# Performance work log

Hardware: AMD Instinct MI355X
Metric: run time of the kernel (lower is better)

The kernel has to match this reference:

```python
import jax, jax.numpy as jnp
import numpy as np

N_NODES = 50000
N_EDGES = 800000
D_IN = 128
D_OUT = 128


def setup_inputs() -> dict:
    key = jax.random.key(0)
    k1, k2, k3, k4 = jax.random.split(key, 4)
    feature = jax.random.normal(k1, (N_NODES, D_IN), dtype=jnp.float32)
    edge_src = jax.random.randint(k2, (N_EDGES,), 0, N_NODES, dtype=jnp.int32)
    edge_dst = jax.random.randint(k3, (N_EDGES,), 0, N_NODES, dtype=jnp.int32)
    W = jax.random.normal(k4, (D_IN, D_OUT), dtype=jnp.float32) * (1.0 / np.sqrt(D_IN))
    b = jnp.zeros((D_OUT,), dtype=jnp.float32)
    return {"feature": feature, "edge_src": edge_src, "edge_dst": edge_dst, "W": W, "b": b}


def reference(feature, edge_src, edge_dst, W, b):
    # copy_src + sum reduce: for each edge, copy src node feature, sum into dst node
    msgs = feature[edge_src]  # [E, D_IN] gather
    h = jax.ops.segment_sum(msgs, edge_dst, num_segments=N_NODES)  # [N, D_IN]
    # linear + activation (relu)
    return jax.nn.relu(h @ W + b)
```

## Files before the change

### kernel.cpp

```cpp
#include <hip/hip_runtime.h>
#include <hip/hip_fp16.h>


constexpr int N    = 50000;
constexpr int E    = 800000;
constexpr int D    = 128;
constexpr int CAP  = 64;
constexpr int NT   = 3125;
constexpr int ZSTR = 136;
constexpr int NR   = 782;
constexpr int HB   = 500;
constexpr int EPB  = E / HB;

using f16x8 = __attribute__((ext_vector_type(8))) _Float16;
using f32x4 = __attribute__((ext_vector_type(4))) float;

__global__ void setup(const float* __restrict__ W, _Float16* __restrict__ Wf,
                      _Float16* __restrict__ Z) {
    if (blockIdx.x == 8) {
        if (threadIdx.x < D) Z[(size_t)N * D + threadIdx.x] = (_Float16)0.f;
        return;
    }
    int t = blockIdx.x * 256 + threadIdx.x;
    int ct = t >> 8, ks = (t >> 6) & 3, lane = t & 63;
    int q = lane >> 4, li = lane & 15;
    _Float16 v[8];
    #pragma unroll
    for (int j = 0; j < 8; ++j)
        v[j] = (_Float16)W[(ks * 32 + q * 8 + j) * D + ct * 16 + li];
    *(f16x8*)(Wf + (size_t)t * 8) = *(const f16x8*)v;
}

__global__ __launch_bounds__(256) void midk(
        const float* __restrict__ feature,
        const int*   __restrict__ edst,
        const _Float16* __restrict__ Wf,
        int* __restrict__ hist,
        _Float16* __restrict__ Z) {
    __shared__ int h[NR];
    __shared__ _Float16 zs[4][16 * ZSTR];
    const int tid = threadIdx.x;

    if (blockIdx.x < HB) {
        const int b = blockIdx.x;
        for (int i = tid; i < NR; i += 256) h[i] = 0;
        __syncthreads();
        const int e0 = b * EPB;
        for (int i = tid; i < EPB; i += 256)
            atomicAdd(&h[edst[e0 + i] >> 6], 1);
        __syncthreads();
        for (int i = tid; i < NR; i += 256) hist[b * NR + i] = h[i];
        return;
    }

    const int wave = tid >> 6, lane = tid & 63;
    const int wt = (blockIdx.x - HB) * 4 + wave;
    if (wt >= NT) return;
    const int q = lane >> 4, li = lane & 15;

    const float* fp = feature + (size_t)(wt * 16 + li) * D + q * 8;
    f16x8 afr[4];
    #pragma unroll
    for (int ks = 0; ks < 4; ++ks) {
        const float4 u0 = *(const float4*)(fp + ks * 32);
        const float4 u1 = *(const float4*)(fp + ks * 32 + 4);
        afr[ks][0] = (_Float16)u0.x; afr[ks][1] = (_Float16)u0.y;
        afr[ks][2] = (_Float16)u0.z; afr[ks][3] = (_Float16)u0.w;
        afr[ks][4] = (_Float16)u1.x; afr[ks][5] = (_Float16)u1.y;
        afr[ks][6] = (_Float16)u1.z; afr[ks][7] = (_Float16)u1.w;
    }

    f32x4 acc[8];
    #pragma unroll
    for (int ct = 0; ct < 8; ++ct) acc[ct] = (f32x4){0.f, 0.f, 0.f, 0.f};
    #pragma unroll
    for (int ks = 0; ks < 4; ++ks)
        #pragma unroll
        for (int ct = 0; ct < 8; ++ct) {
            const f16x8 b = *(const f16x8*)(Wf + (size_t)((ct * 4 + ks) * 64 + lane) * 8);
            acc[ct] = __builtin_amdgcn_mfma_f32_16x16x32_f16(afr[ks], b, acc[ct], 0, 0, 0);
        }

    _Float16* zt = zs[wave];
    #pragma unroll
    for (int ct = 0; ct < 8; ++ct)
        #pragma unroll
        for (int r = 0; r < 4; ++r)
            zt[(q * 4 + r) * ZSTR + ct * 16 + li] = (_Float16)acc[ct][r];
    #pragma unroll
    for (int it = 0; it < 4; ++it) {
        const f16x8 v = *(const f16x8*)(zt + (it * 4 + q) * ZSTR + li * 8);
        *(f16x8*)(Z + (size_t)(wt * 16 + it * 4 + q) * D + li * 8) = v;
    }
}

__global__ void scank(int* __restrict__ hist, int* __restrict__ total) {
    const int r    = blockIdx.x;
    const int lane = threadIdx.x;
    int h[8], sum = 0;
    #pragma unroll
    for (int j = 0; j < 8; ++j) {
        const int idx = lane * 8 + j;
        h[j] = (idx < HB) ? hist[idx * NR + r] : 0;
        sum += h[j];
    }
    int incl = sum;
    #pragma unroll
    for (int off = 1; off < 64; off <<= 1) {
        int u = __shfl_up(incl, off);
        if (lane >= off) incl += u;
    }
    int run = incl - sum;
    #pragma unroll
    for (int j = 0; j < 8; ++j) {
        const int idx = lane * 8 + j;
        if (idx < HB) hist[idx * NR + r] = run;
        run += h[j];
    }
    if (lane == 63) total[r] = run;
}

__global__ __launch_bounds__(256) void partk(
        const int* __restrict__ esrc,
        const int* __restrict__ edst,
        const int* __restrict__ blockBase,
        const int* __restrict__ total,
        int* __restrict__ rangeStartG,
        unsigned int* __restrict__ part) {
    __shared__ int rs[NR];
    __shared__ int mb[NR];
    __shared__ int rk[NR];
    const int tid = threadIdx.x;
    const int b   = blockIdx.x;

    if (tid < 64) {
        int carry = 0;
        #pragma unroll
        for (int c = 0; c < 13; ++c) {
            const int idx = c * 64 + tid;
            const int v = (idx < NR) ? total[idx] : 0;
            int incl = v;
            #pragma unroll
            for (int off = 1; off < 64; off <<= 1) {
                int u = __shfl_up(incl, off);
                if (tid >= off) incl += u;
            }
            if (idx < NR) rs[idx] = incl - v + carry;
            carry += __shfl(incl, 63);
        }
    }
    for (int i = tid; i < NR; i += 256) { mb[i] = blockBase[b * NR + i]; rk[i] = 0; }
    __syncthreads();
    if (b == 0)
        for (int i = tid; i < NR; i += 256) rangeStartG[i] = rs[i];

    const int e0 = b * EPB;
    for (int i = tid; i < EPB; i += 256) {
        const int s = esrc[e0 + i];
        const int d = edst[e0 + i];
        const int r = d >> 6;
        const int k = atomicAdd(&rk[r], 1);
        part[rs[r] + mb[r] + k] = ((unsigned)(d & 63) << 16) | (unsigned)s;
    }
}

__global__ __launch_bounds__(256) void csrgather(
        const unsigned int* __restrict__ part,
        const int* __restrict__ rangeStart,
        const int* __restrict__ total,
        const _Float16* __restrict__ Z,
        const float* __restrict__ bias,
        float* __restrict__ out) {
    __shared__ unsigned short bkt[32 * CAP];
    __shared__ int deg[32];
    const int r   = blockIdx.x >> 1;
    const int sub = blockIdx.x & 1;
    const int tid = threadIdx.x;

    if (tid < 32) deg[tid] = 0;
    __syncthreads();
    const int rsv = rangeStart[r], tot = total[r];
    for (int i = tid; i < tot; i += 256) {
        const unsigned p = part[rsv + i];
        const int local = p >> 16;
        if ((local >> 5) == sub) {
            const int l5 = local & 31;
            const int k = atomicAdd(&deg[l5], 1);
            if (k < CAP) bkt[l5 * CAP + k] = (unsigned short)(p & 0xFFFF);
        }
    }
    __syncthreads();

    const int wave = tid >> 6, lane = tid & 63;
    const int g = lane >> 4, li = lane & 15;
    const float4 b0 = *(const float4*)(bias + li * 8);
    const float4 b1 = *(const float4*)(bias + li * 8 + 4);

    for (int pair = 0; pair < 4; ++pair) {
        const int lA = wave * 8 + pair * 2;
        const int lB = lA + 1;
        const int degA = min(deg[lA], CAP);
        const int degB = min(deg[lB], CAP);

        float accA[8] = {0,0,0,0,0,0,0,0};
        float accB[8] = {0,0,0,0,0,0,0,0};

        const int mx = max(degA, degB);
        for (int base = 0; base < mx; base += 16) {
            f16x8 hA[4], hB[4];
            #pragma unroll
            for (int t = 0; t < 4; ++t) {
                const int rr = base + t * 4 + g;
                int sA = bkt[lA * CAP + rr];
                int sB = bkt[lB * CAP + rr];
                sA = (rr < degA) ? sA : N;
                sB = (rr < degB) ? sB : N;
                hA[t] = *(const f16x8*)(Z + (size_t)sA * D + li * 8);
                hB[t] = *(const f16x8*)(Z + (size_t)sB * D + li * 8);
            }
            #pragma unroll
            for (int t = 0; t < 4; ++t)
                #pragma unroll
                for (int j = 0; j < 8; ++j) {
                    accA[j] += (float)hA[t][j];
                    accB[j] += (float)hB[t][j];
                }
        }

        #pragma unroll
        for (int j = 0; j < 8; ++j) {
            accA[j] += __shfl_xor(accA[j], 16);
            accA[j] += __shfl_xor(accA[j], 32);
            accB[j] += __shfl_xor(accB[j], 16);
            accB[j] += __shfl_xor(accB[j], 32);
        }

        const int nodeA = (r << 6) + (sub << 5) + lA;
        const int nodeB = nodeA + 1;
        if (g == 0 && nodeA < N) {
            float4 o0, o1;
            o0.x = fmaxf(accA[0] + b0.x, 0.f); o0.y = fmaxf(accA[1] + b0.y, 0.f);
            o0.z = fmaxf(accA[2] + b0.z, 0.f); o0.w = fmaxf(accA[3] + b0.w, 0.f);
            o1.x = fmaxf(accA[4] + b1.x, 0.f); o1.y = fmaxf(accA[5] + b1.y, 0.f);
            o1.z = fmaxf(accA[6] + b1.z, 0.f); o1.w = fmaxf(accA[7] + b1.w, 0.f);
            float* op = out + (size_t)nodeA * D + li * 8;
            *(float4*)op       = o0;
            *(float4*)(op + 4) = o1;
        } else if (g == 1 && nodeB < N) {
            float4 o0, o1;
            o0.x = fmaxf(accB[0] + b0.x, 0.f); o0.y = fmaxf(accB[1] + b0.y, 0.f);
            o0.z = fmaxf(accB[2] + b0.z, 0.f); o0.w = fmaxf(accB[3] + b0.w, 0.f);
            o1.x = fmaxf(accB[4] + b1.x, 0.f); o1.y = fmaxf(accB[5] + b1.y, 0.f);
            o1.z = fmaxf(accB[6] + b1.z, 0.f); o1.w = fmaxf(accB[7] + b1.w, 0.f);
            float* op = out + (size_t)nodeB * D + li * 8;
            *(float4*)op       = o0;
            *(float4*)(op + 4) = o1;
        }
    }
}

extern "C" void kernel_launch(void* const* d_in, const int* in_sizes, int n_in,
                              void* d_out, int out_size, void* d_ws, size_t ws_size,
                              hipStream_t stream) {
    const float* feature = (const float*)d_in[0];
    const int*   esrc    = (const int*)d_in[1];
    const int*   edst    = (const int*)d_in[2];
    const float* W       = (const float*)d_in[3];
    const float* bias    = (const float*)d_in[4];
    float*       out     = (float*)d_out;

    _Float16*     Z      = (_Float16*)d_ws;
    _Float16*     Wf     = Z + (size_t)(N + 1) * D;
    int*          hist   = (int*)(Wf + 16384);
    int*          total  = hist + HB * NR;
    int*          rangeS = total + NR;
    unsigned int* part   = (unsigned int*)(rangeS + NR);

    setup<<<9, 256, 0, stream>>>(W, Wf, Z);
    midk <<<HB + (NT + 3) / 4, 256, 0, stream>>>(feature, edst, Wf, hist, Z);
    scank<<<NR, 64, 0, stream>>>(hist, total);
    partk<<<HB, 256, 0, stream>>>(esrc, edst, hist, total, rangeS, part);
    csrgather<<<NR * 2, 256, 0, stream>>>(part, rangeS, total, Z, bias, out);
}
```

Before: 142.0 us.

## Regroup kernels so the GEMM overlaps partitioning and split gather blocks finer

The pipeline is reorganised into four kernels instead of five. The W-conversion setup is folded into the histogram kernel, and the dense feature·W MFMA tiles now run in the same launch as the edge partition scatter, so the compute-heavy GEMM overlaps the atomic-heavy partitioning. The histogram is stored transposed so the scan reads it coalesced, and the scan writes its offsets to a separate array. The gather kernel splits each 64-node range into 4 blocks instead of 2, giving more blocks with less work each, but every block rescans the range's full edge list, so total redundant reads of part increase.

```diff
diff --git a/kernel.cpp b/kernel.cpp
--- a/kernel.cpp
+++ b/kernel.cpp
@@ -11,50 +11,123 @@
 constexpr int NR   = 782;
 constexpr int HB   = 500;
 constexpr int EPB  = E / HB;
+constexpr int SUB  = 4;
 
 using f16x8 = __attribute__((ext_vector_type(8))) _Float16;
 using f32x4 = __attribute__((ext_vector_type(4))) float;
 
-__global__ void setup(const float* __restrict__ W, _Float16* __restrict__ Wf,
-                      _Float16* __restrict__ Z) {
-    if (blockIdx.x == 8) {
-        if (threadIdx.x < D) Z[(size_t)N * D + threadIdx.x] = (_Float16)0.f;
+__device__ __forceinline__ int wscan_incl(int v, int lane) {
+    #pragma unroll
+    for (int off = 1; off < 64; off <<= 1) {
+        int u = __shfl_up(v, off);
+        if (lane >= off) v += u;
+    }
+    return v;
+}
+
+__global__ __launch_bounds__(256) void histk(
+        const int* __restrict__ edst,
+        const float* __restrict__ W,
+        _Float16* __restrict__ Wf,
+        _Float16* __restrict__ Z,
+        int* __restrict__ histT) {
+    __shared__ int h[NR];
+    const int tid = threadIdx.x;
+    const int b   = blockIdx.x;
+
+    if (b >= HB) {
+        if (b == HB + 8) {
+            if (tid < D) Z[(size_t)N * D + tid] = (_Float16)0.f;
+            return;
+        }
+        int t = (b - HB) * 256 + tid;
+        int ct = t >> 8, ks = (t >> 6) & 3, lane = t & 63;
+        int q = lane >> 4, li = lane & 15;
+        _Float16 v[8];
+        #pragma unroll
+        for (int j = 0; j < 8; ++j)
+            v[j] = (_Float16)W[(ks * 32 + q * 8 + j) * D + ct * 16 + li];
+        *(f16x8*)(Wf + (size_t)t * 8) = *(const f16x8*)v;
         return;
     }
-    int t = blockIdx.x * 256 + threadIdx.x;
-    int ct = t >> 8, ks = (t >> 6) & 3, lane = t & 63;
-    int q = lane >> 4, li = lane & 15;
-    _Float16 v[8];
-    #pragma unroll
-    for (int j = 0; j < 8; ++j)
-        v[j] = (_Float16)W[(ks * 32 + q * 8 + j) * D + ct * 16 + li];
-    *(f16x8*)(Wf + (size_t)t * 8) = *(const f16x8*)v;
-}
-
-__global__ __launch_bounds__(256) void midk(
+
+    for (int i = tid; i < NR; i += 256) h[i] = 0;
+    __syncthreads();
+    const int e0 = b * EPB;
+    for (int i = tid; i < EPB; i += 256)
+        atomicAdd(&h[edst[e0 + i] >> 6], 1);
+    __syncthreads();
+    for (int i = tid; i < NR; i += 256) histT[i * HB + b] = h[i];
+}
+
+__global__ void scank(const int* __restrict__ histT,
+                      int* __restrict__ mb,
+                      int* __restrict__ total) {
+    const int r    = blockIdx.x;
+    const int lane = threadIdx.x;
+    int carry = 0;
+    #pragma unroll
+    for (int j = 0; j < 8; ++j) {
+        const int idx = j * 64 + lane;
+        const int v = (idx < HB) ? histT[r * HB + idx] : 0;
+        const int incl = wscan_incl(v, lane);
+        if (idx < HB) mb[idx * NR + r] = incl - v + carry;
+        carry += __shfl(incl, 63);
+    }
+    if (lane == 0) total[r] = carry;
+}
+
+__global__ __launch_bounds__(256) void workk(
         const float* __restrict__ feature,
+        const int*   __restrict__ esrc,
         const int*   __restrict__ edst,
         const _Float16* __restrict__ Wf,
-        int* __restrict__ hist,
+        const int* __restrict__ mb,
+        const int* __restrict__ total,
+        int* __restrict__ rangeStartG,
+        unsigned int* __restrict__ part,
         _Float16* __restrict__ Z) {
-    __shared__ int h[NR];
-    __shared__ _Float16 zs[4][16 * ZSTR];
+    __shared__ union {
+        struct { int rs[NR]; int mbs[NR]; int rk[NR]; } p;
+        _Float16 zs[4][16 * ZSTR];
+    } sh;
     const int tid = threadIdx.x;
-
-    if (blockIdx.x < HB) {
-        const int b = blockIdx.x;
-        for (int i = tid; i < NR; i += 256) h[i] = 0;
+    const int b   = blockIdx.x;
+
+    if (b < HB) {
+        if (tid < 64) {
+            int carry = 0;
+            #pragma unroll
+            for (int c = 0; c < 13; ++c) {
+                const int idx = c * 64 + tid;
+                const int v = (idx < NR) ? total[idx] : 0;
+                const int incl = wscan_incl(v, tid);
+                if (idx < NR) sh.p.rs[idx] = incl - v + carry;
+                carry += __shfl(incl, 63);
+            }
+        }
+        for (int i = tid; i < NR; i += 256) {
+            sh.p.mbs[i] = mb[b * NR + i];
+            sh.p.rk[i]  = 0;
+        }
         __syncthreads();
+        if (b == 0)
+            for (int i = tid; i < NR; i += 256) rangeStartG[i] = sh.p.rs[i];
+
         const int e0 = b * EPB;
-        for (int i = tid; i < EPB; i += 256)
-            atomicAdd(&h[edst[e0 + i] >> 6], 1);
-        __syncthreads();
-        for (int i = tid; i < NR; i += 256) hist[b * NR + i] = h[i];
+        for (int i = tid; i < EPB; i += 256) {
+            const int s = esrc[e0 + i];
+            const int d = edst[e0 + i];
+            const int r = d >> 6;
+            const int k = atomicAdd(&sh.p.rk[r], 1);
+            part[sh.p.rs[r] + sh.p.mbs[r] + k] =
+                ((unsigned)(d & 63) << 16) | (unsigned)s;
+        }
         return;
     }
 
     const int wave = tid >> 6, lane = tid & 63;
-    const int wt = (blockIdx.x - HB) * 4 + wave;
+    const int wt = (b - HB) * 4 + wave;
     if (wt >= NT) return;
     const int q = lane >> 4, li = lane & 15;
 
@@ -77,11 +150,11 @@
     for (int ks = 0; ks < 4; ++ks)
         #pragma unroll
         for (int ct = 0; ct < 8; ++ct) {
-            const f16x8 b = *(const f16x8*)(Wf + (size_t)((ct * 4 + ks) * 64 + lane) * 8);
-            acc[ct] = __builtin_amdgcn_mfma_f32_16x16x32_f16(afr[ks], b, acc[ct], 0, 0, 0);
-        }
-
-    _Float16* zt = zs[wave];
+            const f16x8 bb = *(const f16x8*)(Wf + (size_t)((ct * 4 + ks) * 64 + lane) * 8);
+            acc[ct] = __builtin_amdgcn_mfma_f32_16x16x32_f16(afr[ks], bb, acc[ct], 0, 0, 0);
+        }
+
+    _Float16* zt = sh.zs[wave];
     #pragma unroll
     for (int ct = 0; ct < 8; ++ct)
         #pragma unroll
@@ -91,76 +164,6 @@
     for (int it = 0; it < 4; ++it) {
         const f16x8 v = *(const f16x8*)(zt + (it * 4 + q) * ZSTR + li * 8);
         *(f16x8*)(Z + (size_t)(wt * 16 + it * 4 + q) * D + li * 8) = v;
-    }
-}
-
-__global__ void scank(int* __restrict__ hist, int* __restrict__ total) {
-    const int r    = blockIdx.x;
-    const int lane = threadIdx.x;
-    int h[8], sum = 0;
-    #pragma unroll
-    for (int j = 0; j < 8; ++j) {
-        const int idx = lane * 8 + j;
-        h[j] = (idx < HB) ? hist[idx * NR + r] : 0;
-        sum += h[j];
-    }
-    int incl = sum;
-    #pragma unroll
-    for (int off = 1; off < 64; off <<= 1) {
-        int u = __shfl_up(incl, off);
-        if (lane >= off) incl += u;
-    }
-    int run = incl - sum;
-    #pragma unroll
-    for (int j = 0; j < 8; ++j) {
-        const int idx = lane * 8 + j;
-        if (idx < HB) hist[idx * NR + r] = run;
-        run += h[j];
-    }
-    if (lane == 63) total[r] = run;
-}
-
-__global__ __launch_bounds__(256) void partk(
-        const int* __restrict__ esrc,
-        const int* __restrict__ edst,
-        const int* __restrict__ blockBase,
-        const int* __restrict__ total,
-        int* __restrict__ rangeStartG,
-        unsigned int* __restrict__ part) {
-    __shared__ int rs[NR];
-    __shared__ int mb[NR];
-    __shared__ int rk[NR];
-    const int tid = threadIdx.x;
-    const int b   = blockIdx.x;
-
-    if (tid < 64) {
-        int carry = 0;
-        #pragma unroll
-        for (int c = 0; c < 13; ++c) {
-            const int idx = c * 64 + tid;
-            const int v = (idx < NR) ? total[idx] : 0;
-            int incl = v;
-            #pragma unroll
-            for (int off = 1; off < 64; off <<= 1) {
-                int u = __shfl_up(incl, off);
-                if (tid >= off) incl += u;
-            }
-            if (idx < NR) rs[idx] = incl - v + carry;
-            carry += __shfl(incl, 63);
-        }
-    }
-    for (int i = tid; i < NR; i += 256) { mb[i] = blockBase[b * NR + i]; rk[i] = 0; }
-    __syncthreads();
-    if (b == 0)
-        for (int i = tid; i < NR; i += 256) rangeStartG[i] = rs[i];
-
-    const int e0 = b * EPB;
-    for (int i = tid; i < EPB; i += 256) {
-        const int s = esrc[e0 + i];
-        const int d = edst[e0 + i];
-        const int r = d >> 6;
-        const int k = atomicAdd(&rk[r], 1);
-        part[rs[r] + mb[r] + k] = ((unsigned)(d & 63) << 16) | (unsigned)s;
     }
 }
 
@@ -171,22 +174,22 @@
         const _Float16* __restrict__ Z,
         const float* __restrict__ bias,
         float* __restrict__ out) {
-    __shared__ unsigned short bkt[32 * CAP];
-    __shared__ int deg[32];
-    const int r   = blockIdx.x >> 1;
-    const int sub = blockIdx.x & 1;
+    __shared__ unsigned short bkt[16 * CAP];
+    __shared__ int deg[16];
+    const int r   = blockIdx.x >> 2;
+    const int sub = blockIdx.x & 3;
     const int tid = threadIdx.x;
 
-    if (tid < 32) deg[tid] = 0;
+    if (tid < 16) deg[tid] = 0;
     __syncthreads();
     const int rsv = rangeStart[r], tot = total[r];
     for (int i = tid; i < tot; i += 256) {
         const unsigned p = part[rsv + i];
         const int local = p >> 16;
-        if ((local >> 5) == sub) {
-            const int l5 = local & 31;
-            const int k = atomicAdd(&deg[l5], 1);
-            if (k < CAP) bkt[l5 * CAP + k] = (unsigned short)(p & 0xFFFF);
+        if ((local >> 4) == sub) {
+            const int l4 = local & 15;
+            const int k = atomicAdd(&deg[l4], 1);
+            if (k < CAP) bkt[l4 * CAP + k] = (unsigned short)(p & 0xFFFF);
         }
     }
     __syncthreads();
@@ -196,8 +199,8 @@
     const float4 b0 = *(const float4*)(bias + li * 8);
     const float4 b1 = *(const float4*)(bias + li * 8 + 4);
 
-    for (int pair = 0; pair < 4; ++pair) {
-        const int lA = wave * 8 + pair * 2;
+    for (int pair = 0; pair < 2; ++pair) {
+        const int lA = wave * 4 + pair * 2;
         const int lB = lA + 1;
         const int degA = min(deg[lA], CAP);
         const int degB = min(deg[lB], CAP);
@@ -235,7 +238,7 @@
             accB[j] += __shfl_xor(accB[j], 32);
         }
 
-        const int nodeA = (r << 6) + (sub << 5) + lA;
+        const int nodeA = (r << 6) + (sub << 4) + lA;
         const int nodeB = nodeA + 1;
         if (g == 0 && nodeA < N) {
             float4 o0, o1;
@@ -271,14 +274,15 @@
 
     _Float16*     Z      = (_Float16*)d_ws;
     _Float16*     Wf     = Z + (size_t)(N + 1) * D;
-    int*          hist   = (int*)(Wf + 16384);
-    int*          total  = hist + HB * NR;
+    int*          histT  = (int*)(Wf + 16384);
+    int*          mb     = histT + (size_t)NR * HB;
+    int*          total  = mb + (size_t)HB * NR;
     int*          rangeS = total + NR;
     unsigned int* part   = (unsigned int*)(rangeS + NR);
 
-    setup<<<9, 256, 0, stream>>>(W, Wf, Z);
-    midk <<<HB + (NT + 3) / 4, 256, 0, stream>>>(feature, edst, Wf, hist, Z);
-    scank<<<NR, 64, 0, stream>>>(hist, total);
-    partk<<<HB, 256, 0, stream>>>(esrc, edst, hist, total, rangeS, part);
-    csrgather<<<NR * 2, 256, 0, stream>>>(part, rangeS, total, Z, bias, out);
-}
+    histk<<<HB + 9, 256, 0, stream>>>(edst, W, Wf, Z, histT);
+    scank<<<NR, 64, 0, stream>>>(histT, mb, total);
+    workk<<<HB + (NT + 3) / 4, 256, 0, stream>>>(feature, esrc, edst, Wf,
+                                                 mb, total, rangeS, part, Z);
+    csrgather<<<NR * SUB, 256, 0, stream>>>(part, rangeS, total, Z, bias, out);
+}
```

After: 150.2 us. +5.8%, slower.
